# Kernel tuning notes

Measured on AMD Instinct MI355X. Metric: run time of the kernel, lower is better.

The kernel has to match this reference:

```python
import jax, jax.numpy as jnp
import numpy as np

PS = 8  # window_size
LOCAL = 16  # split channels

def conv1x1(x, w, b):
    return jnp.einsum('oi,bihw->bohw', w, x) + b[None, :, None, None]

def dynamic_local(x, w1, b1, w2, b2, k):
    # x: (B, C, H, W); dynamic per-(batch,channel) depthwise conv with generated kernels
    B, C, H, W = x.shape
    pooled = x.mean((2, 3))                      # (B, C) adaptive avg pool to 1x1
    h = jax.nn.relu(pooled @ w1.T + b1)
    kern = (h @ w2.T + b2).reshape(B, C, k, k)   # per-sample depthwise kernels
    def per_batch(xb, kb):
        return jax.lax.conv_general_dilated(
            xb[None], kb[:, None], (1, 1), 'SAME',
            feature_group_count=C,
            dimension_numbers=('NCHW', 'OIHW', 'NCHW'))[0]
    return jax.vmap(per_batch)(x, kern)

def channel_layernorm(x, w, b, eps=1e-6):
    # LayerNorm over channel dim (torch module's non-channels_last path)
    u = x.mean(1, keepdims=True)
    s = ((x - u) ** 2).mean(1, keepdims=True)
    xn = (x - u) / jnp.sqrt(s + eps)
    return w[None, :, None, None] * xn + b[None, :, None, None]

def fsas(x, hid_w, hid_b, dw_w, dw_b, ln_w, ln_b, out_w, out_b):
    hidden = conv1x1(x, hid_w, hid_b)
    mid = hidden.shape[1]
    dw = jax.lax.conv_general_dilated(
        hidden, dw_w[:, None], (1, 1), 'SAME',
        feature_group_count=mid,
        dimension_numbers=('NCHW', 'OIHW', 'NCHW')) + dw_b[None, :, None, None]
    q, k, v = jnp.split(dw, 3, axis=1)
    B, C, H, W = q.shape
    def patch(t):
        # (B,C,H,W) -> (B,C,H/ps,W/ps,ps,ps)
        return t.reshape(B, C, H // PS, PS, W // PS, PS).transpose(0, 1, 2, 4, 3, 5)
    qf = jnp.fft.rfft2(patch(q))
    kf = jnp.fft.rfft2(patch(k))
    out = jnp.fft.irfft2(qf * kf, s=(PS, PS))
    out = out.transpose(0, 1, 2, 4, 3, 5).reshape(B, C, H, W)
    out = channel_layernorm(out, ln_w, ln_b)
    return conv1x1(v * out, out_w, out_b)


def setup_inputs() -> dict:
    key = jax.random.key(0)
    ks = jax.random.split(key, 12)
    s = 0.02
    return {
        'x': jax.random.normal(ks[0], (4, 64, 256, 256), jnp.float32),
        'dl1_w1': jax.random.normal(ks[1], (16, 16), jnp.float32) * s,
        'dl1_b1': jnp.zeros((16,), jnp.float32),
        'dl1_w2': jax.random.normal(ks[2], (144, 16), jnp.float32) * s,
        'dl1_b2': jnp.zeros((144,), jnp.float32),
        'dl2_w1': jax.random.normal(ks[3], (16, 16), jnp.float32) * s,
        'dl2_b1': jnp.zeros((16,), jnp.float32),
        'dl2_w2': jax.random.normal(ks[4], (400, 16), jnp.float32) * s,
        'dl2_b2': jnp.zeros((400,), jnp.float32),
        'fs_hid_w': jax.random.normal(ks[5], (144, 48), jnp.float32) * s,
        'fs_hid_b': jnp.zeros((144,), jnp.float32),
        'fs_dw_w': jax.random.normal(ks[6], (144, 3, 3), jnp.float32) * s,
        'fs_dw_b': jnp.zeros((144,), jnp.float32),
        'fs_ln_w': jnp.ones((48,), jnp.float32),
        'fs_ln_b': jnp.zeros((48,), jnp.float32),
        'fs_out_w': jax.random.normal(ks[7], (48, 48), jnp.float32) * s,
        'fs_out_b': jnp.zeros((48,), jnp.float32),
        'last_w': jax.random.normal(ks[8], (64, 64), jnp.float32) * s,
        'last_b': jnp.zeros((64,), jnp.float32),
    }


def reference(x, dl1_w1, dl1_b1, dl1_w2, dl1_b2, dl2_w1, dl2_b1, dl2_w2, dl2_b2,
              fs_hid_w, fs_hid_b, fs_dw_w, fs_dw_b, fs_ln_w, fs_ln_b,
              fs_out_w, fs_out_b, last_w, last_b):
    x1, x2 = x[:, :LOCAL], x[:, LOCAL:]
    x1 = dynamic_local(x1, dl1_w1, dl1_b1, dl1_w2, dl1_b2, 3)
    x1 = dynamic_local(x1, dl2_w1, dl2_b1, dl2_w2, dl2_b2, 5)
    x2 = fsas(x2, fs_hid_w, fs_hid_b, fs_dw_w, fs_dw_b, fs_ln_w, fs_ln_b, fs_out_w, fs_out_b)
    return conv1x1(jnp.concatenate([x1, x2], axis=1), last_w, last_b)
```

## Files before the change

### kernel.cpp

```cpp
#include <hip/hip_runtime.h>

typedef _Float16 h2 __attribute__((ext_vector_type(2)));
typedef _Float16 h8 __attribute__((ext_vector_type(8)));
typedef float f4 __attribute__((ext_vector_type(4)));

#if defined(__has_builtin)
#if __has_builtin(__builtin_amdgcn_fdot2)
#define HAS_FDOT2 1
#endif
#endif

__device__ __forceinline__ float warpsum(float v) {
    for (int off = 32; off > 0; off >>= 1) v += __shfl_down(v, off);
    return v;
}

__global__ __launch_bounds__(256) void k_prep(const float* __restrict__ hid_w,
                                              const float* __restrict__ out_w,
                                              const float* __restrict__ last_w,
                                              _Float16* __restrict__ hwH,
                                              _Float16* __restrict__ owlwH) {
    int t = blockIdx.x * 256 + threadIdx.x;
    int stride = gridDim.x * 256;
    for (int i = t; i < 10368; i += stride) {
        int n = i / 72, k = i - n * 72;
        hwH[i] = (k < 48) ? (_Float16)hid_w[n * 48 + k] : (_Float16)0.f;
    }
    for (int i = t; i < 3456; i += stride) {
        int n = i / 72, k = i - n * 72;
        owlwH[i] = (k < 48) ? (_Float16)out_w[n * 48 + k] : (_Float16)0.f;
    }
    for (int i = t; i < 4608; i += stride) {
        int n = i / 72, k = i - n * 72;
        owlwH[3456 + i] = (k < 64) ? (_Float16)last_w[n * 64 + k] : (_Float16)0.f;
    }
}

__global__ __launch_bounds__(256) void k_pool(const float* __restrict__ x, float* __restrict__ pooled1) {
    int bid = blockIdx.x;
    int b = bid >> 4, c = bid & 15;
    const float* base = x + (size_t)(b * 64 + c) * 65536;
    float s = 0.f;
    for (int i = threadIdx.x; i < 16384; i += 256) {
        float4 v = ((const float4*)base)[i];
        s += v.x + v.y + v.z + v.w;
    }
    __shared__ float red[4];
    s = warpsum(s);
    if ((threadIdx.x & 63) == 0) red[threadIdx.x >> 6] = s;
    __syncthreads();
    if (threadIdx.x == 0) pooled1[bid] = (red[0] + red[1] + red[2] + red[3]) * (1.f / 65536.f);
}

__global__ __launch_bounds__(256) void k_kern1(const float* __restrict__ pooled1,
                                               const float* __restrict__ w1, const float* __restrict__ b1,
                                               const float* __restrict__ w2, const float* __restrict__ b2,
                                               float* __restrict__ kern1) {
    __shared__ float h[64];
    int t = threadIdx.x;
    if (t < 64) {
        int b = t >> 4, j = t & 15;
        float a = b1[j];
        for (int i = 0; i < 16; ++i) a += pooled1[b * 16 + i] * w1[j * 16 + i];
        h[t] = fmaxf(a, 0.f);
    }
    __syncthreads();
    for (int i = t; i < 576; i += 256) {
        int b = i / 144, o = i - b * 144;
        float a = b2[o];
        for (int j = 0; j < 16; ++j) a += h[b * 16 + j] * w2[o * 16 + j];
        kern1[i] = a;
    }
}

__global__ __launch_bounds__(256) void k_dw3(const float* __restrict__ x,
                                             const float* __restrict__ kern1,
                                             float* __restrict__ y1, float* __restrict__ rowsum) {
    __shared__ float tile[10][258];
    __shared__ float red[8][4];
    int bid = blockIdx.x;
    int rb = bid & 31, bc = bid >> 5;
    int b = bc >> 4, c = bc & 15;
    int row0 = rb << 3;
    int col = threadIdx.x;
    const float* xc = x + ((size_t)(b * 64 + c) << 16);
#pragma unroll
    for (int j = 0; j < 10; ++j) {
        int r = row0 - 1 + j;
        tile[j][col + 1] = ((unsigned)r < 256u) ? xc[(r << 8) + col] : 0.f;
    }
    if (col < 10) { tile[col][0] = 0.f; tile[col][257] = 0.f; }
    const float* k9 = kern1 + b * 144 + c * 9;
    float kk[9];
#pragma unroll
    for (int i = 0; i < 9; ++i) kk[i] = k9[i];
    __syncthreads();
#pragma unroll
    for (int j = 0; j < 8; ++j) {
        float acc = 0.f;
#pragma unroll
        for (int dy = 0; dy < 3; ++dy)
#pragma unroll
            for (int dx = 0; dx < 3; ++dx)
                acc += kk[dy * 3 + dx] * tile[j + dy][col + dx];
        y1[((size_t)bc << 16) + ((row0 + j) << 8) + col] = acc;
        float s = warpsum(acc);
        if ((col & 63) == 0) red[j][col >> 6] = s;
    }
    __syncthreads();
    if (col < 8) rowsum[bc * 256 + row0 + col] = red[col][0] + red[col][1] + red[col][2] + red[col][3];
}

__global__ __launch_bounds__(256) void k_kern2(const float* __restrict__ rowsum,
                                               const float* __restrict__ w1, const float* __restrict__ b1,
                                               const float* __restrict__ w2, const float* __restrict__ b2,
                                               float* __restrict__ kern2) {
    __shared__ float ps[256];
    __shared__ float p2[64];
    __shared__ float h[64];
    int t = threadIdx.x;
    {
        int pair = t >> 2, seg = t & 3;
        const float* rs = rowsum + pair * 256 + seg * 64;
        float s = 0.f;
        for (int j = 0; j < 64; ++j) s += rs[j];
        ps[t] = s;
    }
    __syncthreads();
    if (t < 64) p2[t] = (ps[t * 4] + ps[t * 4 + 1] + ps[t * 4 + 2] + ps[t * 4 + 3]) * (1.f / 65536.f);
    __syncthreads();
    if (t < 64) {
        int b = t >> 4, j = t & 15;
        float a = b1[j];
        for (int i = 0; i < 16; ++i) a += p2[b * 16 + i] * w1[j * 16 + i];
        h[t] = fmaxf(a, 0.f);
    }
    __syncthreads();
    for (int i = t; i < 1600; i += 256) {
        int b = i / 400, o = i - b * 400;
        float a = b2[o];
        for (int j = 0; j < 16; ++j) a += h[b * 16 + j] * w2[o * 16 + j];
        kern2[i] = a;
    }
}

__global__ __launch_bounds__(256) void k_dw5(const float* __restrict__ y1,
                                             const float* __restrict__ kern2,
                                             float* __restrict__ x1o) {
    __shared__ float tile[12][260];
    int bid = blockIdx.x;
    int rb = bid & 31, bc = bid >> 5;
    int b = bc >> 4, c = bc & 15;
    int row0 = rb << 3;
    int col = threadIdx.x;
    const float* yc = y1 + ((size_t)bc << 16);
#pragma unroll
    for (int j = 0; j < 12; ++j) {
        int r = row0 - 2 + j;
        tile[j][col + 2] = ((unsigned)r < 256u) ? yc[(r << 8) + col] : 0.f;
    }
    if (col < 12) { tile[col][0] = 0.f; tile[col][1] = 0.f; tile[col][258] = 0.f; tile[col][259] = 0.f; }
    const float* k25 = kern2 + b * 400 + c * 25;
    float kk[25];
#pragma unroll
    for (int i = 0; i < 25; ++i) kk[i] = k25[i];
    __syncthreads();
#pragma unroll
    for (int j = 0; j < 8; ++j) {
        float acc = 0.f;
#pragma unroll
        for (int dy = 0; dy < 5; ++dy)
#pragma unroll
            for (int dx = 0; dx < 5; ++dx)
                acc += kk[dy * 5 + dx] * tile[j + dy][col + dx];
        x1o[((size_t)bc << 16) + ((row0 + j) << 8) + col] = acc;
    }
}

__global__ __launch_bounds__(512, 4) void k_fsas(const float* __restrict__ x,
                                                 const _Float16* __restrict__ hwH, const float* __restrict__ hid_b,
                                                 const float* __restrict__ dw_w, const float* __restrict__ dw_b,
                                                 const float* __restrict__ ln_w, const float* __restrict__ ln_b,
                                                 const _Float16* __restrict__ owlwH, const float* __restrict__ out_b,
                                                 const float* __restrict__ last_b,
                                                 const float* __restrict__ x1o, float* __restrict__ out) {
    __shared__ __align__(16) _Float16 Abuf[8064];
    __shared__ __align__(16) _Float16 wbuf[8064];
    __shared__ __align__(16) _Float16 hbuf[4992];
    __shared__ __align__(16) _Float16 qbuf[3456];
    __shared__ __align__(16) _Float16 kbuf2[6528];
    __shared__ __align__(16) float pstat[128];

    _Float16* fbuf  = Abuf;
    float*    lnp   = (float*)(Abuf + 4608);
    _Float16* outb  = hbuf;
    _Float16* cbuf  = hbuf;
    _Float16* sbufA = kbuf2;

    int tid = threadIdx.x;
    int lane = tid & 63;
    int wave = __builtin_amdgcn_readfirstlane(tid >> 6);
    int bid = blockIdx.x;
    int swz = ((bid & 7) << 9) | (bid >> 3);
    int b = swz >> 10;
    int rem = swz & 1023;
    int row0 = (rem >> 5) << 3, col0 = (rem & 31) << 3;

    int px2 = tid & 63, pr = tid >> 6;
    size_t gpix2 = ((size_t)(row0 + (px2 >> 3)) << 8) + col0 + (px2 & 7);

    for (int j = tid; j < 4032; j += 512) ((unsigned int*)Abuf)[j] = 0u;
    for (int i = tid; i < 1728; i += 512) ((unsigned int*)wbuf)[i] = ((const unsigned int*)hwH)[i];
    __syncthreads();

    for (int j = tid; j < 4800; j += 512) {
        int k = j / 100, p = j - k * 100;
        int yv = p / 10, xv = p - yv * 10;
        int gy = row0 - 1 + yv, gx = col0 - 1 + xv;
        if ((unsigned)gy < 256u && (unsigned)gx < 256u)
            Abuf[p * 72 + k] = (_Float16)x[((size_t)(b * 64 + 16 + k) << 16) + (gy << 8) + gx];
    }
    __syncthreads();

    float vreg[6];
#pragma unroll 1
    for (int ph = 0; ph < 3; ++ph) {
        if (wave < 7) {
            int mt = wave;
            int fr = (lane & 15) * 72 + ((lane >> 4) << 3);
            h8 a0 = *(const h8*)(Abuf + mt * 1152 + fr);
            h8 a1 = *(const h8*)(Abuf + mt * 1152 + 32 + fr);
#pragma unroll
            for (int nt = 0; nt < 3; ++nt) {
                h8 b0 = *(const h8*)(wbuf + nt * 1152 + fr);
                h8 b1 = *(const h8*)(wbuf + nt * 1152 + 32 + fr);
                float bias = hid_b[ph * 48 + nt * 16 + (lane & 15)];
                f4 acc = {bias, bias, bias, bias};
                acc = __builtin_amdgcn_mfma_f32_16x16x32_f16(a0, b0, acc, 0, 0, 0);
                acc = __builtin_amdgcn_mfma_f32_16x16x32_f16(a1, b1, acc, 0, 0, 0);
                int n_l = nt * 16 + (lane & 15);
                int mb = mt * 16 + ((lane >> 4) << 2);
#pragma unroll
                for (int r = 0; r < 4; ++r) {
                    int m = mb + r;
                    if (m < 104) {
                        bool ok = (m < 100);
                        if (ok) {
                            int yv = m / 10, xv = m - yv * 10;
                            ok = ((unsigned)(row0 - 1 + yv) < 256u) && ((unsigned)(col0 - 1 + xv) < 256u);
                        }
                        hbuf[n_l * 104 + m] = ok ? (_Float16)acc[r] : (_Float16)0.f;
                    }
                }
            }
        }
        __syncthreads();
        {
            int yy = lane >> 3, xd = lane & 7;
            int cl0 = wave * 6;
#pragma unroll
            for (int u = 0; u < 6; ++u) {
                int cl = cl0 + u, c = ph * 48 + cl;
                const float* dwp = dw_w + c * 9;
                const _Float16* hb = hbuf + cl * 104 + yy * 10 + xd;
                float a = dw_b[c];
#pragma unroll
                for (int dy = 0; dy < 3; ++dy)
#pragma unroll
                    for (int dx = 0; dx < 3; ++dx)
                        a += dwp[dy * 3 + dx] * (float)hb[dy * 10 + dx];
                if (ph == 0) qbuf[cl * 72 + lane] = (_Float16)a;
                else if (ph == 1) {
                    int jj = lane & 7;
                    kbuf2[cl * 136 + yy * 16 + ((8 - jj) & 7)] = (_Float16)a;
                    kbuf2[cl * 136 + yy * 16 + 8 + ((9 - jj) & 7)] = (_Float16)a;
                } else vreg[u] = a;
            }
        }
        if (ph < 2) {
            const unsigned int* src = (const unsigned int*)(hwH + (ph + 1) * 3456);
            for (int i = tid; i < 1728; i += 512) ((unsigned int*)wbuf)[i] = src[i];
        }
        __syncthreads();
    }

    float xa = x1o[((size_t)(b * 16 + 2 * pr) << 16) + gpix2];
    float xb = x1o[((size_t)(b * 16 + 2 * pr + 1) << 16) + gpix2];

    if (tid < 384) {
        int ch = tid >> 3, m = tid & 7;
        float co[8];
#pragma unroll
        for (int n = 0; n < 8; ++n) co[n] = 0.f;
#pragma unroll
        for (int i8 = 0; i8 < 8; ++i8) {
            int r = (m - i8) & 7;
            h8 q8 = *(const h8*)(qbuf + ch * 72 + i8 * 8);
            h8 e8 = *(const h8*)(kbuf2 + ch * 136 + r * 16);
#ifdef HAS_FDOT2
            h8 o8 = *(const h8*)(kbuf2 + ch * 136 + r * 16 + 8);
            h2 qp[4], ep[4], op[4];
            qp[0] = __builtin_shufflevector(q8, q8, 0, 1); qp[1] = __builtin_shufflevector(q8, q8, 2, 3);
            qp[2] = __builtin_shufflevector(q8, q8, 4, 5); qp[3] = __builtin_shufflevector(q8, q8, 6, 7);
            ep[0] = __builtin_shufflevector(e8, e8, 0, 1); ep[1] = __builtin_shufflevector(e8, e8, 2, 3);
            ep[2] = __builtin_shufflevector(e8, e8, 4, 5); ep[3] = __builtin_shufflevector(e8, e8, 6, 7);
            op[0] = __builtin_shufflevector(o8, o8, 0, 1); op[1] = __builtin_shufflevector(o8, o8, 2, 3);
            op[2] = __builtin_shufflevector(o8, o8, 4, 5); op[3] = __builtin_shufflevector(o8, o8, 6, 7);
#pragma unroll
            for (int u = 0; u < 4; ++u)
#pragma unroll
                for (int a = 0; a < 4; ++a) {
                    co[2 * u]     = __builtin_amdgcn_fdot2(qp[a], ep[(a - u) & 3], co[2 * u], false);
                    co[2 * u + 1] = __builtin_amdgcn_fdot2(qp[a], op[(a - u) & 3], co[2 * u + 1], false);
                }
#else
            float qf[8], kf[8];
#pragma unroll
            for (int j = 0; j < 8; ++j) { qf[j] = (float)q8[j]; kf[j] = (float)e8[(8 - j) & 7]; }
#pragma unroll
            for (int j = 0; j < 8; ++j)
#pragma unroll
                for (int n = 0; n < 8; ++n)
                    co[n] += qf[j] * kf[(n - j) & 7];
#endif
        }
#pragma unroll
        for (int v = 0; v < 4; ++v)
            *(h2*)(outb + ch * 72 + m * 8 + 2 * v) = (h2){(_Float16)co[2 * v], (_Float16)co[2 * v + 1]};
    } else {
        for (int j = tid - 384; j < 4032; j += 128)
            ((unsigned int*)wbuf)[j] = ((const unsigned int*)owlwH)[j];
    }
    *(h2*)(fbuf + px2 * 72 + 2 * pr) = (h2){(_Float16)xa, (_Float16)xb};
    __syncthreads();

    {
        float s = 0.f, ss = 0.f;
#pragma unroll
        for (int cc = 0; cc < 6; ++cc) {
            float v = (float)outb[(pr * 6 + cc) * 72 + px2];
            s += v; ss += v * v;
        }
        lnp[pr * 64 + px2] = s;
        lnp[512 + pr * 64 + px2] = ss;
    }
    __syncthreads();
    if (tid < 64) {
        float s = 0.f, ss = 0.f;
#pragma unroll
        for (int g = 0; g < 8; ++g) { s += lnp[g * 64 + tid]; ss += lnp[512 + g * 64 + tid]; }
        float mu = s * (1.f / 48.f);
        float var = ss * (1.f / 48.f) - mu * mu;
        pstat[tid * 2] = mu;
        pstat[tid * 2 + 1] = rsqrtf(var + 1e-6f);
    }
    __syncthreads();

    {
        float mu = pstat[lane * 2], inv = pstat[lane * 2 + 1];
        int cl0 = wave * 6;
#pragma unroll
        for (int u = 0; u < 6; ++u) {
            int cl = cl0 + u;
            float o = (float)outb[cl * 72 + lane];
            float lnv = ln_w[cl] * ((o - mu) * inv) + ln_b[cl];
            sbufA[lane * 72 + cl] = (_Float16)(vreg[u] * lnv);
        }
        *(h2*)(sbufA + px2 * 72 + 48 + 2 * pr) = (h2){(_Float16)0.f, (_Float16)0.f};
    }
    __syncthreads();

    for (int t = wave; t < 12; t += 8) {
        int mt = t / 3, nt = t - mt * 3;
        int fr = (lane & 15) * 72 + ((lane >> 4) << 3);
        h8 a0 = *(const h8*)(sbufA + mt * 1152 + fr);
        h8 a1 = *(const h8*)(sbufA + mt * 1152 + 32 + fr);
        h8 b0 = *(const h8*)(wbuf + nt * 1152 + fr);
        h8 b1 = *(const h8*)(wbuf + nt * 1152 + 32 + fr);
        float bias = out_b[nt * 16 + (lane & 15)];
        f4 acc = {bias, bias, bias, bias};
        acc = __builtin_amdgcn_mfma_f32_16x16x32_f16(a0, b0, acc, 0, 0, 0);
        acc = __builtin_amdgcn_mfma_f32_16x16x32_f16(a1, b1, acc, 0, 0, 0);
        int n5 = nt * 16 + (lane & 15);
        int pb = mt * 16 + ((lane >> 4) << 2);
#pragma unroll
        for (int r = 0; r < 4; ++r)
            fbuf[(pb + r) * 72 + 16 + n5] = (_Float16)acc[r];
    }
    __syncthreads();

    for (int t = wave; t < 16; t += 8) {
        int mt = t >> 2, nt = t & 3;
        int fr = (lane & 15) * 72 + ((lane >> 4) << 3);
        h8 a0 = *(const h8*)(fbuf + mt * 1152 + fr);
        h8 a1 = *(const h8*)(fbuf + mt * 1152 + 32 + fr);
        h8 b0 = *(const h8*)(wbuf + 3456 + nt * 1152 + fr);
        h8 b1 = *(const h8*)(wbuf + 3456 + nt * 1152 + 32 + fr);
        float bias = last_b[nt * 16 + (lane & 15)];
        f4 acc = {bias, bias, bias, bias};
        acc = __builtin_amdgcn_mfma_f32_16x16x32_f16(a0, b0, acc, 0, 0, 0);
        acc = __builtin_amdgcn_mfma_f32_16x16x32_f16(a1, b1, acc, 0, 0, 0);
        int ch = nt * 16 + (lane & 15);
        int pb = mt * 16 + ((lane >> 4) << 2);
#pragma unroll
        for (int r = 0; r < 4; ++r)
            cbuf[ch * 72 + pb + r] = (_Float16)acc[r];
    }
    __syncthreads();

#pragma unroll
    for (int u = 0; u < 8; ++u) {
        int ch = pr * 8 + u;
        out[((size_t)(b * 64 + ch) << 16) + gpix2] = (float)cbuf[ch * 72 + px2];
    }
}

extern "C" void kernel_launch(void* const* d_in, const int* in_sizes, int n_in,
                              void* d_out, int out_size, void* d_ws, size_t ws_size,
                              hipStream_t stream) {
    const float* x      = (const float*)d_in[0];
    const float* dl1_w1 = (const float*)d_in[1];
    const float* dl1_b1 = (const float*)d_in[2];
    const float* dl1_w2 = (const float*)d_in[3];
    const float* dl1_b2 = (const float*)d_in[4];
    const float* dl2_w1 = (const float*)d_in[5];
    const float* dl2_b1 = (const float*)d_in[6];
    const float* dl2_w2 = (const float*)d_in[7];
    const float* dl2_b2 = (const float*)d_in[8];
    const float* hid_w  = (const float*)d_in[9];
    const float* hid_b  = (const float*)d_in[10];
    const float* dw_w   = (const float*)d_in[11];
    const float* dw_b   = (const float*)d_in[12];
    const float* ln_w   = (const float*)d_in[13];
    const float* ln_b   = (const float*)d_in[14];
    const float* out_w  = (const float*)d_in[15];
    const float* out_b  = (const float*)d_in[16];
    const float* last_w = (const float*)d_in[17];
    const float* last_b = (const float*)d_in[18];
    float* out = (float*)d_out;

    float* ws      = (float*)d_ws;
    float* pooled1 = ws;
    float* kern1   = ws + 64;
    float* rowsum  = ws + 1024;
    float* kern2   = ws + 17408;
    _Float16* hwH   = (_Float16*)(ws + 19008);
    _Float16* owlwH = (_Float16*)(ws + 24192);
    float* y1      = ws + 32768;
    float* x1o     = ws + 32768 + 4194304;

    k_prep <<<8,    256, 0, stream>>>(hid_w, out_w, last_w, hwH, owlwH);
    k_pool <<<64,   256, 0, stream>>>(x, pooled1);
    k_kern1<<<1,    256, 0, stream>>>(pooled1, dl1_w1, dl1_b1, dl1_w2, dl1_b2, kern1);
    k_dw3  <<<2048, 256, 0, stream>>>(x, kern1, y1, rowsum);
    k_kern2<<<1,    256, 0, stream>>>(rowsum, dl2_w1, dl2_b1, dl2_w2, dl2_b2, kern2);
    k_dw5  <<<2048, 256, 0, stream>>>(y1, kern2, x1o);
    k_fsas <<<4096, 512, 0, stream>>>(x, hwH, hid_b, dw_w, dw_b, ln_w, ln_b,
                                      owlwH, out_b, last_b, x1o, out);
}
```

Before: 204.4 us.

## Drop shared weight buffer, read MFMA weights from global, restructure depthwise conv

Removes the shared-memory weight buffer and loads the hidden, out and last projection weights directly from global memory (cached) into MFMA operands, which cuts LDS usage and raises the occupancy hint to 6 blocks per CU. The halo tile is padded to a 12-wide pitch so all 8 waves do MFMA work. The depthwise 3x3 conv is rewritten so each thread produces a row of 8 outputs from vectorized LDS loads. The v tensor now goes to an LDS buffer instead of registers. The trade-off is more global or L2 weight traffic and tighter register limits in exchange for higher occupancy and fewer barriers or copies.

```diff
diff --git a/kernel.cpp b/kernel.cpp
--- a/kernel.cpp
+++ b/kernel.cpp
@@ -1,6 +1,7 @@
 #include <hip/hip_runtime.h>
 
 typedef _Float16 h2 __attribute__((ext_vector_type(2)));
+typedef _Float16 h4 __attribute__((ext_vector_type(4)));
 typedef _Float16 h8 __attribute__((ext_vector_type(8)));
 typedef float f4 __attribute__((ext_vector_type(4)));
 
@@ -177,22 +178,22 @@
     }
 }
 
-__global__ __launch_bounds__(512, 4) void k_fsas(const float* __restrict__ x,
+__global__ __launch_bounds__(512, 6) void k_fsas(const float* __restrict__ x,
                                                  const _Float16* __restrict__ hwH, const float* __restrict__ hid_b,
                                                  const float* __restrict__ dw_w, const float* __restrict__ dw_b,
                                                  const float* __restrict__ ln_w, const float* __restrict__ ln_b,
                                                  const _Float16* __restrict__ owlwH, const float* __restrict__ out_b,
                                                  const float* __restrict__ last_b,
                                                  const float* __restrict__ x1o, float* __restrict__ out) {
-    __shared__ __align__(16) _Float16 Abuf[8064];
-    __shared__ __align__(16) _Float16 wbuf[8064];
-    __shared__ __align__(16) _Float16 hbuf[4992];
+    __shared__ __align__(16) _Float16 Abuf[10368];
+    __shared__ __align__(16) _Float16 hbuf[5760];
     __shared__ __align__(16) _Float16 qbuf[3456];
     __shared__ __align__(16) _Float16 kbuf2[6528];
     __shared__ __align__(16) float pstat[128];
 
     _Float16* fbuf  = Abuf;
     float*    lnp   = (float*)(Abuf + 4608);
+    _Float16* vbuf  = Abuf + 6656;
     _Float16* outb  = hbuf;
     _Float16* cbuf  = hbuf;
     _Float16* sbufA = kbuf2;
@@ -206,80 +207,101 @@
     int rem = swz & 1023;
     int row0 = (rem >> 5) << 3, col0 = (rem & 31) << 3;
 
-    int px2 = tid & 63, pr = tid >> 6;
+    int px2 = lane, pr = wave;
     size_t gpix2 = ((size_t)(row0 + (px2 >> 3)) << 8) + col0 + (px2 & 7);
 
-    for (int j = tid; j < 4032; j += 512) ((unsigned int*)Abuf)[j] = 0u;
-    for (int i = tid; i < 1728; i += 512) ((unsigned int*)wbuf)[i] = ((const unsigned int*)hwH)[i];
+    int l16 = lane & 15, lhi = lane >> 4;
+    int fr = l16 * 72 + (lhi << 3);
+    int mb = wave * 16 + (lhi << 2);
+    bool st[4], vok[4];
+#pragma unroll
+    for (int r = 0; r < 4; ++r) {
+        int m = mb + r;
+        st[r] = (m < 120);
+        int yv = m / 12, xv = m - yv * 12;
+        vok[r] = st[r] && (xv < 10) &&
+                 ((unsigned)(row0 - 1 + yv) < 256u) && ((unsigned)(col0 - 1 + xv) < 256u);
+    }
+
+    for (int j = tid; j < 4608; j += 512) ((unsigned int*)Abuf)[j] = 0u;
     __syncthreads();
 
     for (int j = tid; j < 4800; j += 512) {
-        int k = j / 100, p = j - k * 100;
-        int yv = p / 10, xv = p - yv * 10;
+        int k = j / 100, q = j - k * 100;
+        int yv = q / 10, xv = q - yv * 10;
         int gy = row0 - 1 + yv, gx = col0 - 1 + xv;
         if ((unsigned)gy < 256u && (unsigned)gx < 256u)
-            Abuf[p * 72 + k] = (_Float16)x[((size_t)(b * 64 + 16 + k) << 16) + (gy << 8) + gx];
-    }
-    __syncthreads();
-
-    float vreg[6];
+            Abuf[(yv * 12 + xv) * 72 + k] = (_Float16)x[((size_t)(b * 64 + 16 + k) << 16) + (gy << 8) + gx];
+    }
+    __syncthreads();
+
+    h8 a0 = *(const h8*)(Abuf + wave * 1152 + fr);
+    h8 a1 = *(const h8*)(Abuf + wave * 1152 + 32 + fr);
+
+    int dch = tid >> 3, drow = tid & 7;
+
 #pragma unroll 1
     for (int ph = 0; ph < 3; ++ph) {
-        if (wave < 7) {
-            int mt = wave;
-            int fr = (lane & 15) * 72 + ((lane >> 4) << 3);
-            h8 a0 = *(const h8*)(Abuf + mt * 1152 + fr);
-            h8 a1 = *(const h8*)(Abuf + mt * 1152 + 32 + fr);
-#pragma unroll
-            for (int nt = 0; nt < 3; ++nt) {
-                h8 b0 = *(const h8*)(wbuf + nt * 1152 + fr);
-                h8 b1 = *(const h8*)(wbuf + nt * 1152 + 32 + fr);
-                float bias = hid_b[ph * 48 + nt * 16 + (lane & 15)];
-                f4 acc = {bias, bias, bias, bias};
-                acc = __builtin_amdgcn_mfma_f32_16x16x32_f16(a0, b0, acc, 0, 0, 0);
-                acc = __builtin_amdgcn_mfma_f32_16x16x32_f16(a1, b1, acc, 0, 0, 0);
-                int n_l = nt * 16 + (lane & 15);
-                int mb = mt * 16 + ((lane >> 4) << 2);
-#pragma unroll
-                for (int r = 0; r < 4; ++r) {
-                    int m = mb + r;
-                    if (m < 104) {
-                        bool ok = (m < 100);
-                        if (ok) {
-                            int yv = m / 10, xv = m - yv * 10;
-                            ok = ((unsigned)(row0 - 1 + yv) < 256u) && ((unsigned)(col0 - 1 + xv) < 256u);
-                        }
-                        hbuf[n_l * 104 + m] = ok ? (_Float16)acc[r] : (_Float16)0.f;
-                    }
+        const _Float16* wp = hwH + ph * 3456;
+        h8 b0[3], b1[3];
+#pragma unroll
+        for (int nt = 0; nt < 3; ++nt) {
+            b0[nt] = *(const h8*)(wp + nt * 1152 + fr);
+            b1[nt] = *(const h8*)(wp + nt * 1152 + 32 + fr);
+        }
+#pragma unroll
+        for (int nt = 0; nt < 3; ++nt) {
+            float bias = hid_b[ph * 48 + nt * 16 + l16];
+            f4 acc = {bias, bias, bias, bias};
+            acc = __builtin_amdgcn_mfma_f32_16x16x32_f16(a0, b0[nt], acc, 0, 0, 0);
+            acc = __builtin_amdgcn_mfma_f32_16x16x32_f16(a1, b1[nt], acc, 0, 0, 0);
+            int n_l = nt * 16 + l16;
+#pragma unroll
+            for (int r = 0; r < 4; ++r)
+                if (st[r]) hbuf[n_l * 120 + mb + r] = vok[r] ? (_Float16)acc[r] : (_Float16)0.f;
+        }
+        __syncthreads();
+        if (tid < 384) {
+            int c = ph * 48 + dch;
+            const float* dwp = dw_w + c * 9;
+            float bias = dw_b[c];
+            float o[8];
+#pragma unroll
+            for (int xx = 0; xx < 8; ++xx) o[xx] = bias;
+            const _Float16* hb = hbuf + dch * 120 + drow * 12;
+#pragma unroll
+            for (int dy = 0; dy < 3; ++dy) {
+                h4 r0 = *(const h4*)(hb + dy * 12);
+                h4 r1 = *(const h4*)(hb + dy * 12 + 4);
+                h2 r2 = *(const h2*)(hb + dy * 12 + 8);
+                float rowv[10] = {(float)r0[0], (float)r0[1], (float)r0[2], (float)r0[3],
+                                  (float)r1[0], (float)r1[1], (float)r1[2], (float)r1[3],
+                                  (float)r2[0], (float)r2[1]};
+                float w0 = dwp[dy * 3], w1 = dwp[dy * 3 + 1], w2 = dwp[dy * 3 + 2];
+#pragma unroll
+                for (int xx = 0; xx < 8; ++xx)
+                    o[xx] += w0 * rowv[xx] + w1 * rowv[xx + 1] + w2 * rowv[xx + 2];
+            }
+            if (ph == 0) {
+                h8 qv;
+#pragma unroll
+                for (int xx = 0; xx < 8; ++xx) qv[xx] = (_Float16)o[xx];
+                *(h8*)(qbuf + dch * 72 + drow * 8) = qv;
+            } else if (ph == 1) {
+                h8 kr, ko;
+#pragma unroll
+                for (int t2 = 0; t2 < 8; ++t2) {
+                    kr[t2] = (_Float16)o[(8 - t2) & 7];
+                    ko[t2] = (_Float16)o[(9 - t2) & 7];
                 }
+                *(h8*)(kbuf2 + dch * 136 + drow * 16) = kr;
+                *(h8*)(kbuf2 + dch * 136 + drow * 16 + 8) = ko;
+            } else {
+                h8 vv;
+#pragma unroll
+                for (int xx = 0; xx < 8; ++xx) vv[xx] = (_Float16)o[xx];
+                *(h8*)(vbuf + dch * 72 + drow * 8) = vv;
             }
-        }
-        __syncthreads();
-        {
-            int yy = lane >> 3, xd = lane & 7;
-            int cl0 = wave * 6;
-#pragma unroll
-            for (int u = 0; u < 6; ++u) {
-                int cl = cl0 + u, c = ph * 48 + cl;
-                const float* dwp = dw_w + c * 9;
-                const _Float16* hb = hbuf + cl * 104 + yy * 10 + xd;
-                float a = dw_b[c];
-#pragma unroll
-                for (int dy = 0; dy < 3; ++dy)
-#pragma unroll
-                    for (int dx = 0; dx < 3; ++dx)
-                        a += dwp[dy * 3 + dx] * (float)hb[dy * 10 + dx];
-                if (ph == 0) qbuf[cl * 72 + lane] = (_Float16)a;
-                else if (ph == 1) {
-                    int jj = lane & 7;
-                    kbuf2[cl * 136 + yy * 16 + ((8 - jj) & 7)] = (_Float16)a;
-                    kbuf2[cl * 136 + yy * 16 + 8 + ((9 - jj) & 7)] = (_Float16)a;
-                } else vreg[u] = a;
-            }
-        }
-        if (ph < 2) {
-            const unsigned int* src = (const unsigned int*)(hwH + (ph + 1) * 3456);
-            for (int i = tid; i < 1728; i += 512) ((unsigned int*)wbuf)[i] = src[i];
         }
         __syncthreads();
     }
@@ -327,9 +349,6 @@
 #pragma unroll
         for (int v = 0; v < 4; ++v)
             *(h2*)(outb + ch * 72 + m * 8 + 2 * v) = (h2){(_Float16)co[2 * v], (_Float16)co[2 * v + 1]};
-    } else {
-        for (int j = tid - 384; j < 4032; j += 128)
-            ((unsigned int*)wbuf)[j] = ((const unsigned int*)owlwH)[j];
     }
     *(h2*)(fbuf + px2 * 72 + 2 * pr) = (h2){(_Float16)xa, (_Float16)xb};
     __syncthreads();
@@ -363,8 +382,9 @@
         for (int u = 0; u < 6; ++u) {
             int cl = cl0 + u;
             float o = (float)outb[cl * 72 + lane];
+            float vv = (float)vbuf[cl * 72 + lane];
             float lnv = ln_w[cl] * ((o - mu) * inv) + ln_b[cl];
-            sbufA[lane * 72 + cl] = (_Float16)(vreg[u] * lnv);
+            sbufA[lane * 72 + cl] = (_Float16)(vv * lnv);
         }
         *(h2*)(sbufA + px2 * 72 + 48 + 2 * pr) = (h2){(_Float16)0.f, (_Float16)0.f};
     }
@@ -372,17 +392,16 @@
 
     for (int t = wave; t < 12; t += 8) {
         int mt = t / 3, nt = t - mt * 3;
-        int fr = (lane & 15) * 72 + ((lane >> 4) << 3);
-        h8 a0 = *(const h8*)(sbufA + mt * 1152 + fr);
-        h8 a1 = *(const h8*)(sbufA + mt * 1152 + 32 + fr);
-        h8 b0 = *(const h8*)(wbuf + nt * 1152 + fr);
-        h8 b1 = *(const h8*)(wbuf + nt * 1152 + 32 + fr);
-        float bias = out_b[nt * 16 + (lane & 15)];
+        h8 c0 = *(const h8*)(sbufA + mt * 1152 + fr);
+        h8 c1 = *(const h8*)(sbufA + mt * 1152 + 32 + fr);
+        h8 d0 = *(const h8*)(owlwH + nt * 1152 + fr);
+        h8 d1 = *(const h8*)(owlwH + nt * 1152 + 32 + fr);
+        float bias = out_b[nt * 16 + l16];
         f4 acc = {bias, bias, bias, bias};
-        acc = __builtin_amdgcn_mfma_f32_16x16x32_f16(a0, b0, acc, 0, 0, 0);
-        acc = __builtin_amdgcn_mfma_f32_16x16x32_f16(a1, b1, acc, 0, 0, 0);
-        int n5 = nt * 16 + (lane & 15);
-        int pb = mt * 16 + ((lane >> 4) << 2);
+        acc = __builtin_amdgcn_mfma_f32_16x16x32_f16(c0, d0, acc, 0, 0, 0);
+        acc = __builtin_amdgcn_mfma_f32_16x16x32_f16(c1, d1, acc, 0, 0, 0);
+        int n5 = nt * 16 + l16;
+        int pb = mt * 16 + (lhi << 2);
 #pragma unroll
         for (int r = 0; r < 4; ++r)
             fbuf[(pb + r) * 72 + 16 + n5] = (_Float16)acc[r];
@@ -391,17 +410,16 @@
 
     for (int t = wave; t < 16; t += 8) {
         int mt = t >> 2, nt = t & 3;
-        int fr = (lane & 15) * 72 + ((lane >> 4) << 3);
-        h8 a0 = *(const h8*)(fbuf + mt * 1152 + fr);
-        h8 a1 = *(const h8*)(fbuf + mt * 1152 + 32 + fr);
-        h8 b0 = *(const h8*)(wbuf + 3456 + nt * 1152 + fr);
-        h8 b1 = *(const h8*)(wbuf + 3456 + nt * 1152 + 32 + fr);
-        float bias = last_b[nt * 16 + (lane & 15)];
+        h8 c0 = *(const h8*)(fbuf + mt * 1152 + fr);
+        h8 c1 = *(const h8*)(fbuf + mt * 1152 + 32 + fr);
+        h8 d0 = *(const h8*)(owlwH + 3456 + nt * 1152 + fr);
+        h8 d1 = *(const h8*)(owlwH + 3456 + nt * 1152 + 32 + fr);
+        float bias = last_b[nt * 16 + l16];
         f4 acc = {bias, bias, bias, bias};
-        acc = __builtin_amdgcn_mfma_f32_16x16x32_f16(a0, b0, acc, 0, 0, 0);
-        acc = __builtin_amdgcn_mfma_f32_16x16x32_f16(a1, b1, acc, 0, 0, 0);
-        int ch = nt * 16 + (lane & 15);
-        int pb = mt * 16 + ((lane >> 4) << 2);
+        acc = __builtin_amdgcn_mfma_f32_16x16x32_f16(c0, d0, acc, 0, 0, 0);
+        acc = __builtin_amdgcn_mfma_f32_16x16x32_f16(c1, d1, acc, 0, 0, 0);
+        int ch = nt * 16 + l16;
+        int pb = mt * 16 + (lhi << 2);
 #pragma unroll
         for (int r = 0; r < 4; ++r)
             cbuf[ch * 72 + pb + r] = (_Float16)acc[r];
```

After: 179.8 us. 12.0% less time.
